# Performance work log

Measured on AMD Instinct MI355X. Metric: run time of the kernel, lower is better.

The kernel has to match this reference:

```python
import jax, jax.numpy as jnp
import numpy as np

N_POINTS = 200
LEVEL_DIM = 4
NUM_LEVELS = 3
RESOLUTIONS = (8, 16, 32)  # base_resolution=8, per-level scale 2
BATCH = 32768


def _sph_to_cart(theta, phi):
    st = jnp.sin(theta)
    return jnp.stack([st * jnp.cos(phi), st * jnp.sin(phi), jnp.cos(theta)], axis=-1)


def _sample_points(x):
    # x: [B,4] -> points on segment between two unit-sphere points: [B, N_POINTS, 3]
    p1 = _sph_to_cart(x[:, 0], x[:, 1])
    p2 = _sph_to_cart(x[:, 2], x[:, 3])
    t = jnp.linspace(0.0, 1.0, N_POINTS, dtype=x.dtype).reshape(1, N_POINTS, 1)
    return p1[:, None, :] + (p2 - p1)[:, None, :] * t


def _grid_interp(points, table, R):
    # points: [B,S,3] in [-1,1]; table: [(R+1)^3, D] dense grid. Trilinear interp.
    u = jnp.clip((points + 1.0) * 0.5, 0.0, 1.0) * R
    p0 = jnp.clip(jnp.floor(u).astype(jnp.int32), 0, R - 1)
    f = u - p0.astype(u.dtype)
    Rp1 = R + 1
    out = jnp.zeros(points.shape[:-1] + (table.shape[-1],), dtype=table.dtype)
    for c in range(8):  # fixed 8 trilinear corners
        off = np.array([(c >> 2) & 1, (c >> 1) & 1, c & 1], dtype=np.int32)
        idx = p0 + off
        lin = (idx[..., 0] * Rp1 + idx[..., 1]) * Rp1 + idx[..., 2]
        w = jnp.prod(jnp.where(off == 1, f, 1.0 - f), axis=-1)
        out = out + w[..., None] * table[lin]
    return out


def setup_inputs() -> dict:
    key = jax.random.key(0)
    ks = jax.random.split(key, 8)
    pi = 3.14159265
    x = jax.random.uniform(ks[0], (BATCH, 4), dtype=jnp.float32) * pi
    grid0 = jax.random.normal(ks[1], ((RESOLUTIONS[0] + 1) ** 3, LEVEL_DIM), jnp.float32) * 0.1
    grid1 = jax.random.normal(ks[2], ((RESOLUTIONS[1] + 1) ** 3, LEVEL_DIM), jnp.float32) * 0.1
    grid2 = jax.random.normal(ks[3], ((RESOLUTIONS[2] + 1) ** 3, LEVEL_DIM), jnp.float32) * 0.1
    w_label = jax.random.normal(ks[4], (NUM_LEVELS, 1), jnp.float32) * 0.5
    b_label = jnp.zeros((1,), jnp.float32)
    w_rgb = jax.random.normal(ks[5], (NUM_LEVELS * (LEVEL_DIM - 1), 3), jnp.float32) * 0.3
    b_rgb = jnp.zeros((3,), jnp.float32)
    return {"x": x, "grid0": grid0, "grid1": grid1, "grid2": grid2,
            "w_label": w_label, "b_label": b_label, "w_rgb": w_rgb, "b_rgb": b_rgb}


def reference(x, grid0, grid1, grid2, w_label, b_label, w_rgb, b_rgb):
    # torch wraps ray sampling in no_grad -> stop_gradient
    points = jax.lax.stop_gradient(_sample_points(x))  # [B,S,3]
    enc = jnp.concatenate(
        [_grid_interp(points, g, R) for g, R in zip((grid0, grid1, grid2), RESOLUTIONS)],
        axis=-1)  # [B,S,12]
    labels_in = enc[:, :, ::LEVEL_DIM]                      # [B,S,3]
    all_prob = jax.nn.sigmoid(labels_in @ w_label + b_label)  # [B,S,1]
    output_hits = jnp.max(all_prob, axis=1)                 # [B,1]
    mask = np.ones(NUM_LEVELS * LEVEL_DIM, dtype=bool)
    mask[::LEVEL_DIM] = False
    rgb_feats = enc[:, :, mask]                             # [B,S,9]
    hit = (all_prob > 0.5).astype(enc.dtype)
    idx_first = jnp.argmax(hit, axis=1)                     # [B,1] first sample with prob>0.5 (0 if none)
    idx3 = jnp.broadcast_to(idx_first[:, :, None], (rgb_feats.shape[0], 1, rgb_feats.shape[2]))
    gathered = jnp.take_along_axis(rgb_feats, idx3, axis=1)[:, 0, :]  # [B,9]
    output_rgb = jax.nn.sigmoid(gathered @ w_rgb + b_rgb)   # [B,3]
    return (output_hits, output_rgb)
```

## Files before the change

### kernel.cpp

```cpp
#include <hip/hip_runtime.h>
#include <math.h>

#define NPTS 200
#define L33   33
#define L33SQ 1089
#define NLAT  35937

template<int R>
__device__ __forceinline__ float tri_label(const float* __restrict__ g,
                                           float ux, float uy, float uz) {
    constexpr int Rp1 = R + 1;
    constexpr int SX  = Rp1 * Rp1;
    int ix = min((int)ux, R - 1);
    int iy = min((int)uy, R - 1);
    int iz = min((int)uz, R - 1);
    float fx = ux - (float)ix, fy = uy - (float)iy, fz = uz - (float)iz;
    int b = (ix * Rp1 + iy) * Rp1 + iz;
    float v000 = g[4*b],            v001 = g[4*(b+1)];
    float v010 = g[4*(b+Rp1)],      v011 = g[4*(b+Rp1+1)];
    float v100 = g[4*(b+SX)],       v101 = g[4*(b+SX+1)];
    float v110 = g[4*(b+SX+Rp1)],   v111 = g[4*(b+SX+Rp1+1)];
    float c00 = fmaf(fz, v001 - v000, v000);
    float c01 = fmaf(fz, v011 - v010, v010);
    float c10 = fmaf(fz, v101 - v100, v100);
    float c11 = fmaf(fz, v111 - v110, v110);
    float c0  = fmaf(fy, c01 - c00, c00);
    float c1  = fmaf(fy, c11 - c10, c10);
    return fmaf(fx, c1 - c0, c0);
}

__device__ __forceinline__ float T_eval(const float* __restrict__ g0,
                                        const float* __restrict__ g1,
                                        const float* __restrict__ g2,
                                        float wl0, float wl1, float wl2, float bl0,
                                        int jx, int jy, int jz) {
    float fx = (float)jx, fy = (float)jy, fz = (float)jz;
    float L0 = tri_label<8 >(g0, fx * 0.25f, fy * 0.25f, fz * 0.25f);
    float L1 = tri_label<16>(g1, fx * 0.5f,  fy * 0.5f,  fz * 0.5f);
    float L2 = g2[4 * ((jx * L33 + jy) * L33 + jz)];
    return bl0 + wl0 * L0 + wl1 * L1 + wl2 * L2;
}

__global__ __launch_bounds__(256)
void prep_kernel(const float* __restrict__ g0, const float* __restrict__ g1,
                 const float* __restrict__ g2, const float* __restrict__ wl,
                 const float* __restrict__ bl, float4* __restrict__ P) {
    int i = blockIdx.x * blockDim.x + threadIdx.x;
    if (i >= NLAT) return;
    int iz = i % L33;
    int r  = i / L33;
    int iy = r % L33;
    int ix = r / L33;
    int izp = min(iz + 1, L33 - 1);
    int iyp = min(iy + 1, L33 - 1);
    float wl0 = wl[0], wl1 = wl[1], wl2 = wl[2], bl0 = bl[0];
    float4 v;
    v.x = T_eval(g0, g1, g2, wl0, wl1, wl2, bl0, ix, iy,  iz );
    v.y = T_eval(g0, g1, g2, wl0, wl1, wl2, bl0, ix, iy,  izp);
    v.z = T_eval(g0, g1, g2, wl0, wl1, wl2, bl0, ix, iyp, iz );
    v.w = T_eval(g0, g1, g2, wl0, wl1, wl2, bl0, ix, iyp, izp);
    P[i] = v;
}

template<int R>
__device__ __forceinline__ void rgb_corner(const float* __restrict__ g,
                                           float cx, float cy, float cz,
                                           int dx, int dy, int dz,
                                           float* f3) {
    constexpr int Rp1 = R + 1;
    float ux = cx * (float)R, uy = cy * (float)R, uz = cz * (float)R;
    int ix = min((int)ux, R - 1);
    int iy = min((int)uy, R - 1);
    int iz = min((int)uz, R - 1);
    float fx = ux - (float)ix, fy = uy - (float)iy, fz = uz - (float)iz;
    int idx = ((ix + dx) * Rp1 + (iy + dy)) * Rp1 + (iz + dz);
    float w = (dx ? fx : 1.0f - fx) * (dy ? fy : 1.0f - fy) * (dz ? fz : 1.0f - fz);
    float4 v = *reinterpret_cast<const float4*>(g + 4 * idx);
    f3[0] = w * v.y;
    f3[1] = w * v.z;
    f3[2] = w * v.w;
}

__global__ __launch_bounds__(256)
void rays_kernel(const float* __restrict__ x,
                 const float4* __restrict__ P,
                 const float* __restrict__ g0,
                 const float* __restrict__ g1,
                 const float* __restrict__ g2,
                 const float* __restrict__ wr,
                 const float* __restrict__ br,
                 float* __restrict__ out_hits,
                 float* __restrict__ out_rgb,
                 int n)
{
    const int tid = blockIdx.x * blockDim.x + threadIdx.x;
    const int ray = tid >> 3;
    const int sub = (int)(threadIdx.x & 7);
    if (ray >= n) return;

    const float th1 = x[ray * 4 + 0];
    const float ph1 = x[ray * 4 + 1];
    const float th2 = x[ray * 4 + 2];
    const float ph2 = x[ray * 4 + 3];
    float s1 = __sinf(th1), c1 = __cosf(th1);
    float s2 = __sinf(th2), c2 = __cosf(th2);
    float p1x = s1 * __cosf(ph1), p1y = s1 * __sinf(ph1), p1z = c1;
    float p2x = s2 * __cosf(ph2), p2y = s2 * __sinf(ph2), p2z = c2;
    const float dxr = p2x - p1x, dyr = p2y - p1y, dzr = p2z - p1z;

    const float inv = 1.0f / (float)(NPTS - 1);
    const float sc  = 16.0f * inv;

    const float bx = fmaf(p1x, 16.0f, 16.0f);
    const float by = fmaf(p1y, 16.0f, 16.0f);
    const float bz = fmaf(p1z, 16.0f, 16.0f);
    const float dux = dxr * sc, duy = dyr * sc, duz = dzr * sc;

    float tf = (float)sub;
    float maxlogit = -INFINITY;
    int firsthit = NPTS;

#pragma unroll 5
    for (int i = 0; i < 25; ++i) {
        float ux = fminf(fmaxf(fmaf(tf, dux, bx), 0.0f), 32.0f);
        float uy = fminf(fmaxf(fmaf(tf, duy, by), 0.0f), 32.0f);
        float uz = fminf(fmaxf(fmaf(tf, duz, bz), 0.0f), 32.0f);
        int ix = min((int)ux, 31);
        int iy = min((int)uy, 31);
        int iz = min((int)uz, 31);
        float fx = ux - (float)ix;
        float fy = uy - (float)iy;
        float fz = uz - (float)iz;
        int idx = (ix * L33 + iy) * L33 + iz;
        float4 q0 = P[idx];
        float4 q1 = P[idx + L33SQ];
        float mx = fmaf(fx, q1.x - q0.x, q0.x);
        float my = fmaf(fx, q1.y - q0.y, q0.y);
        float mz = fmaf(fx, q1.z - q0.z, q0.z);
        float mw = fmaf(fx, q1.w - q0.w, q0.w);
        float r0 = fmaf(fz, my - mx, mx);
        float r1 = fmaf(fz, mw - mz, mz);
        float logit = fmaf(fy, r1 - r0, r0);
        maxlogit = fmaxf(maxlogit, logit);
        if (logit > 0.0f) firsthit = min(firsthit, sub + i * 8);
        tf += 8.0f;
    }

#pragma unroll
    for (int m = 4; m >= 1; m >>= 1) {
        maxlogit = fmaxf(maxlogit, __shfl_xor(maxlogit, m, 64));
        firsthit = min(firsthit, __shfl_xor(firsthit, m, 64));
    }

    const int tsel = (firsthit >= NPTS) ? 0 : firsthit;
    {
        float tt = (float)tsel * inv;
        float px = fmaf(dxr, tt, p1x);
        float py = fmaf(dyr, tt, p1y);
        float pz = fmaf(dzr, tt, p1z);
        float cx = fminf(fmaxf(fmaf(px, 0.5f, 0.5f), 0.0f), 1.0f);
        float cy = fminf(fmaxf(fmaf(py, 0.5f, 0.5f), 0.0f), 1.0f);
        float cz = fminf(fmaxf(fmaf(pz, 0.5f, 0.5f), 0.0f), 1.0f);
        const int dx = (sub >> 2) & 1, dy = (sub >> 1) & 1, dz = sub & 1;
        float feat[9];
        rgb_corner<8 >(g0, cx, cy, cz, dx, dy, dz, &feat[0]);
        rgb_corner<16>(g1, cx, cy, cz, dx, dy, dz, &feat[3]);
        rgb_corner<32>(g2, cx, cy, cz, dx, dy, dz, &feat[6]);
#pragma unroll
        for (int m = 4; m >= 1; m >>= 1) {
#pragma unroll
            for (int k = 0; k < 9; ++k)
                feat[k] += __shfl_xor(feat[k], m, 64);
        }
        if (sub == 0) {
            out_hits[ray] = 1.0f / (1.0f + __expf(-maxlogit));
#pragma unroll
            for (int c = 0; c < 3; ++c) {
                float acc = br[c];
#pragma unroll
                for (int f = 0; f < 9; ++f) acc += feat[f] * wr[f * 3 + c];
                out_rgb[ray * 3 + c] = 1.0f / (1.0f + __expf(-acc));
            }
        }
    }
}

extern "C" void kernel_launch(void* const* d_in, const int* in_sizes, int n_in,
                              void* d_out, int out_size, void* d_ws, size_t ws_size,
                              hipStream_t stream) {
    const float* x  = (const float*)d_in[0];
    const float* g0 = (const float*)d_in[1];
    const float* g1 = (const float*)d_in[2];
    const float* g2 = (const float*)d_in[3];
    const float* wl = (const float*)d_in[4];
    const float* bl = (const float*)d_in[5];
    const float* wr = (const float*)d_in[6];
    const float* br = (const float*)d_in[7];

    const int n = in_sizes[0] / 4;
    float* out_hits = (float*)d_out;
    float* out_rgb  = (float*)d_out + n;

    float4* P = (float4*)d_ws;

    prep_kernel<<<(NLAT + 255) / 256, 256, 0, stream>>>(g0, g1, g2, wl, bl, P);

    const int block = 256;
    const int grid = (n * 8 + block - 1) / block;
    rays_kernel<<<grid, block, 0, stream>>>(x, P, g0, g1, g2, wr, br,
                                            out_hits, out_rgb, n);
}
```

Before: 21.98 us.

## Store 8-corner label cells and give each thread contiguous samples with cell reuse

Label-logit precompute is split into two kernels. The first evaluates the scalar logit per lattice point, removing the 4x redundant evaluation. The second packs all 8 corners of each 32^3 cell into two float4s. The ray kernel now gives each sub-thread 25 contiguous samples instead of strided ones, so consecutive samples usually land in the same cell and the reload is skipped when the cell index is unchanged. This adds a third kernel launch and a divergent branch, and removes the clamp on sample coordinates since points on the unit sphere stay in range.

Measured after the change: 24.75 us. +12.6%, slower.

```diff
diff --git a/kernel.cpp b/kernel.cpp
--- a/kernel.cpp
+++ b/kernel.cpp
@@ -5,6 +5,8 @@
 #define L33   33
 #define L33SQ 1089
 #define NLAT  35937
+#define NCELL 32768
+#define T_OFF_FLOATS (NCELL * 8)
 
 template<int R>
 __device__ __forceinline__ float tri_label(const float* __restrict__ g,
@@ -29,37 +31,38 @@
     return fmaf(fx, c1 - c0, c0);
 }
 
-__device__ __forceinline__ float T_eval(const float* __restrict__ g0,
-                                        const float* __restrict__ g1,
-                                        const float* __restrict__ g2,
-                                        float wl0, float wl1, float wl2, float bl0,
-                                        int jx, int jy, int jz) {
+__global__ __launch_bounds__(256)
+void prep1_kernel(const float* __restrict__ g0, const float* __restrict__ g1,
+                  const float* __restrict__ g2, const float* __restrict__ wl,
+                  const float* __restrict__ bl, float* __restrict__ T) {
+    int i = blockIdx.x * blockDim.x + threadIdx.x;
+    if (i >= NLAT) return;
+    int jz = i % L33;
+    int r  = i / L33;
+    int jy = r % L33;
+    int jx = r / L33;
     float fx = (float)jx, fy = (float)jy, fz = (float)jz;
     float L0 = tri_label<8 >(g0, fx * 0.25f, fy * 0.25f, fz * 0.25f);
     float L1 = tri_label<16>(g1, fx * 0.5f,  fy * 0.5f,  fz * 0.5f);
-    float L2 = g2[4 * ((jx * L33 + jy) * L33 + jz)];
-    return bl0 + wl0 * L0 + wl1 * L1 + wl2 * L2;
+    float L2 = g2[4 * i];
+    T[i] = bl[0] + wl[0] * L0 + wl[1] * L1 + wl[2] * L2;
 }
 
 __global__ __launch_bounds__(256)
-void prep_kernel(const float* __restrict__ g0, const float* __restrict__ g1,
-                 const float* __restrict__ g2, const float* __restrict__ wl,
-                 const float* __restrict__ bl, float4* __restrict__ P) {
+void prep2_kernel(const float* __restrict__ T, float4* __restrict__ C) {
     int i = blockIdx.x * blockDim.x + threadIdx.x;
-    if (i >= NLAT) return;
-    int iz = i % L33;
-    int r  = i / L33;
-    int iy = r % L33;
-    int ix = r / L33;
-    int izp = min(iz + 1, L33 - 1);
-    int iyp = min(iy + 1, L33 - 1);
-    float wl0 = wl[0], wl1 = wl[1], wl2 = wl[2], bl0 = bl[0];
-    float4 v;
-    v.x = T_eval(g0, g1, g2, wl0, wl1, wl2, bl0, ix, iy,  iz );
-    v.y = T_eval(g0, g1, g2, wl0, wl1, wl2, bl0, ix, iy,  izp);
-    v.z = T_eval(g0, g1, g2, wl0, wl1, wl2, bl0, ix, iyp, iz );
-    v.w = T_eval(g0, g1, g2, wl0, wl1, wl2, bl0, ix, iyp, izp);
-    P[i] = v;
+    if (i >= NCELL) return;
+    int iz = i & 31;
+    int iy = (i >> 5) & 31;
+    int ix = i >> 10;
+    int b = (ix * L33 + iy) * L33 + iz;
+    float4 a, c;
+    a.x = T[b];            a.y = T[b + 1];
+    a.z = T[b + L33];      a.w = T[b + L33 + 1];
+    c.x = T[b + L33SQ];        c.y = T[b + L33SQ + 1];
+    c.z = T[b + L33SQ + L33];  c.w = T[b + L33SQ + L33 + 1];
+    C[2 * i]     = a;
+    C[2 * i + 1] = c;
 }
 
 template<int R>
@@ -83,7 +86,7 @@
 
 __global__ __launch_bounds__(256)
 void rays_kernel(const float* __restrict__ x,
-                 const float4* __restrict__ P,
+                 const float4* __restrict__ C,
                  const float* __restrict__ g0,
                  const float* __restrict__ g1,
                  const float* __restrict__ g2,
@@ -116,24 +119,28 @@
     const float bz = fmaf(p1z, 16.0f, 16.0f);
     const float dux = dxr * sc, duy = dyr * sc, duz = dzr * sc;
 
-    float tf = (float)sub;
+    float tf = (float)(sub * 25);
     float maxlogit = -INFINITY;
     int firsthit = NPTS;
-
-#pragma unroll 5
+    int cidx = -1;
+    float4 q0 = {0.f, 0.f, 0.f, 0.f}, q1 = {0.f, 0.f, 0.f, 0.f};
+
     for (int i = 0; i < 25; ++i) {
-        float ux = fminf(fmaxf(fmaf(tf, dux, bx), 0.0f), 32.0f);
-        float uy = fminf(fmaxf(fmaf(tf, duy, by), 0.0f), 32.0f);
-        float uz = fminf(fmaxf(fmaf(tf, duz, bz), 0.0f), 32.0f);
+        float ux = fmaf(tf, dux, bx);
+        float uy = fmaf(tf, duy, by);
+        float uz = fmaf(tf, duz, bz);
         int ix = min((int)ux, 31);
         int iy = min((int)uy, 31);
         int iz = min((int)uz, 31);
         float fx = ux - (float)ix;
         float fy = uy - (float)iy;
         float fz = uz - (float)iz;
-        int idx = (ix * L33 + iy) * L33 + iz;
-        float4 q0 = P[idx];
-        float4 q1 = P[idx + L33SQ];
+        int idx = (ix << 10) + (iy << 5) + iz;
+        if (idx != cidx) {
+            cidx = idx;
+            q0 = C[2 * idx];
+            q1 = C[2 * idx + 1];
+        }
         float mx = fmaf(fx, q1.x - q0.x, q0.x);
         float my = fmaf(fx, q1.y - q0.y, q0.y);
         float mz = fmaf(fx, q1.z - q0.z, q0.z);
@@ -142,8 +149,8 @@
         float r1 = fmaf(fz, mw - mz, mz);
         float logit = fmaf(fy, r1 - r0, r0);
         maxlogit = fmaxf(maxlogit, logit);
-        if (logit > 0.0f) firsthit = min(firsthit, sub + i * 8);
-        tf += 8.0f;
+        if (logit > 0.0f) firsthit = min(firsthit, sub * 25 + i);
+        tf += 1.0f;
     }
 
 #pragma unroll
@@ -201,12 +208,14 @@
     float* out_hits = (float*)d_out;
     float* out_rgb  = (float*)d_out + n;
 
-    float4* P = (float4*)d_ws;
-
-    prep_kernel<<<(NLAT + 255) / 256, 256, 0, stream>>>(g0, g1, g2, wl, bl, P);
+    float4* C = (float4*)d_ws;
+    float*  T = (float*)d_ws + T_OFF_FLOATS;
+
+    prep1_kernel<<<(NLAT + 255) / 256, 256, 0, stream>>>(g0, g1, g2, wl, bl, T);
+    prep2_kernel<<<(NCELL + 255) / 256, 256, 0, stream>>>(T, C);
 
     const int block = 256;
     const int grid = (n * 8 + block - 1) / block;
-    rays_kernel<<<grid, block, 0, stream>>>(x, P, g0, g1, g2, wr, br,
+    rays_kernel<<<grid, block, 0, stream>>>(x, C, g0, g1, g2, wr, br,
                                             out_hits, out_rgb, n);
 }
```

## Reorder precomputed logit lattice x-fastest and reduce rgb after projection

Applied to the files above, without the earlier changes.

The prep kernel now lays out the label-logit lattice with x as the fastest axis and computes one float per thread, so the two corner loads per sample are adjacent float4s instead of a full plane apart. The sample loop is fully unrolled with per-iteration t, the redundant clamps are dropped, and launch bounds request 4 blocks per CU. The rgb path projects the 9 features onto 3 outputs before the cross-lane shuffle, cutting shuffles from 27 to 9. Dropping the clamp assumes the points stay inside [-1,1], which holds for unit-sphere endpoints but could return slightly different indices at exact boundaries.

New measurement: 21.35 us. 1.03x faster.

```diff
diff --git a/kernel.cpp b/kernel.cpp
--- a/kernel.cpp
+++ b/kernel.cpp
@@ -3,8 +3,8 @@
 
 #define NPTS 200
 #define L33   33
-#define L33SQ 1089
 #define NLAT  35937
+#define NPREP (NLAT * 4)
 
 template<int R>
 __device__ __forceinline__ float tri_label(const float* __restrict__ g,
@@ -29,37 +29,25 @@
     return fmaf(fx, c1 - c0, c0);
 }
 
-__device__ __forceinline__ float T_eval(const float* __restrict__ g0,
-                                        const float* __restrict__ g1,
-                                        const float* __restrict__ g2,
-                                        float wl0, float wl1, float wl2, float bl0,
-                                        int jx, int jy, int jz) {
-    float fx = (float)jx, fy = (float)jy, fz = (float)jz;
-    float L0 = tri_label<8 >(g0, fx * 0.25f, fy * 0.25f, fz * 0.25f);
-    float L1 = tri_label<16>(g1, fx * 0.5f,  fy * 0.5f,  fz * 0.5f);
-    float L2 = g2[4 * ((jx * L33 + jy) * L33 + jz)];
-    return bl0 + wl0 * L0 + wl1 * L1 + wl2 * L2;
-}
-
 __global__ __launch_bounds__(256)
 void prep_kernel(const float* __restrict__ g0, const float* __restrict__ g1,
                  const float* __restrict__ g2, const float* __restrict__ wl,
-                 const float* __restrict__ bl, float4* __restrict__ P) {
-    int i = blockIdx.x * blockDim.x + threadIdx.x;
-    if (i >= NLAT) return;
-    int iz = i % L33;
-    int r  = i / L33;
-    int iy = r % L33;
-    int ix = r / L33;
-    int izp = min(iz + 1, L33 - 1);
-    int iyp = min(iy + 1, L33 - 1);
-    float wl0 = wl[0], wl1 = wl[1], wl2 = wl[2], bl0 = bl[0];
-    float4 v;
-    v.x = T_eval(g0, g1, g2, wl0, wl1, wl2, bl0, ix, iy,  iz );
-    v.y = T_eval(g0, g1, g2, wl0, wl1, wl2, bl0, ix, iy,  izp);
-    v.z = T_eval(g0, g1, g2, wl0, wl1, wl2, bl0, ix, iyp, iz );
-    v.w = T_eval(g0, g1, g2, wl0, wl1, wl2, bl0, ix, iyp, izp);
-    P[i] = v;
+                 const float* __restrict__ bl, float* __restrict__ Pf) {
+    int id = blockIdx.x * blockDim.x + threadIdx.x;
+    if (id >= NPREP) return;
+    int c  = id & 3;
+    int jj = id >> 2;
+    int ix = jj % L33;
+    int r  = jj / L33;
+    int iz = r % L33;
+    int iy = r / L33;
+    int jy = min(iy + (c >> 1), L33 - 1);
+    int jz = min(iz + (c & 1),  L33 - 1);
+    float fx = (float)ix, fy = (float)jy, fz = (float)jz;
+    float L0 = tri_label<8 >(g0, fx * 0.25f, fy * 0.25f, fz * 0.25f);
+    float L1 = tri_label<16>(g1, fx * 0.5f,  fy * 0.5f,  fz * 0.5f);
+    float L2 = g2[4 * ((ix * L33 + jy) * L33 + jz)];
+    Pf[id] = bl[0] + wl[0] * L0 + wl[1] * L1 + wl[2] * L2;
 }
 
 template<int R>
@@ -81,7 +69,7 @@
     f3[2] = w * v.w;
 }
 
-__global__ __launch_bounds__(256)
+__global__ __launch_bounds__(256, 4)
 void rays_kernel(const float* __restrict__ x,
                  const float4* __restrict__ P,
                  const float* __restrict__ g0,
@@ -116,24 +104,26 @@
     const float bz = fmaf(p1z, 16.0f, 16.0f);
     const float dux = dxr * sc, duy = dyr * sc, duz = dzr * sc;
 
-    float tf = (float)sub;
+    const float subf = (float)sub;
     float maxlogit = -INFINITY;
     int firsthit = NPTS;
 
-#pragma unroll 5
+#pragma unroll
     for (int i = 0; i < 25; ++i) {
-        float ux = fminf(fmaxf(fmaf(tf, dux, bx), 0.0f), 32.0f);
-        float uy = fminf(fmaxf(fmaf(tf, duy, by), 0.0f), 32.0f);
-        float uz = fminf(fmaxf(fmaf(tf, duz, bz), 0.0f), 32.0f);
+        float tf = subf + (float)(8 * i);
+        float ux = fmaf(tf, dux, bx);
+        float uy = fmaf(tf, duy, by);
+        float uz = fmaf(tf, duz, bz);
         int ix = min((int)ux, 31);
         int iy = min((int)uy, 31);
         int iz = min((int)uz, 31);
         float fx = ux - (float)ix;
         float fy = uy - (float)iy;
         float fz = uz - (float)iz;
-        int idx = (ix * L33 + iy) * L33 + iz;
-        float4 q0 = P[idx];
-        float4 q1 = P[idx + L33SQ];
+        int jj = (iy * L33 + iz) * L33 + ix;
+        const float4* p = P + jj;
+        float4 q0 = p[0];
+        float4 q1 = p[1];
         float mx = fmaf(fx, q1.x - q0.x, q0.x);
         float my = fmaf(fx, q1.y - q0.y, q0.y);
         float mz = fmaf(fx, q1.z - q0.z, q0.z);
@@ -142,8 +132,7 @@
         float r1 = fmaf(fz, mw - mz, mz);
         float logit = fmaf(fy, r1 - r0, r0);
         maxlogit = fmaxf(maxlogit, logit);
-        if (logit > 0.0f) firsthit = min(firsthit, sub + i * 8);
-        tf += 8.0f;
+        if (logit > 0.0f) firsthit = min(firsthit, 8 * i + sub);
     }
 
 #pragma unroll
@@ -166,21 +155,25 @@
         rgb_corner<8 >(g0, cx, cy, cz, dx, dy, dz, &feat[0]);
         rgb_corner<16>(g1, cx, cy, cz, dx, dy, dz, &feat[3]);
         rgb_corner<32>(g2, cx, cy, cz, dx, dy, dz, &feat[6]);
+        float acc[3];
+#pragma unroll
+        for (int c = 0; c < 3; ++c) {
+            float a = 0.0f;
+#pragma unroll
+            for (int f = 0; f < 9; ++f) a = fmaf(feat[f], wr[f * 3 + c], a);
+            acc[c] = a;
+        }
 #pragma unroll
         for (int m = 4; m >= 1; m >>= 1) {
 #pragma unroll
-            for (int k = 0; k < 9; ++k)
-                feat[k] += __shfl_xor(feat[k], m, 64);
+            for (int c = 0; c < 3; ++c)
+                acc[c] += __shfl_xor(acc[c], m, 64);
         }
         if (sub == 0) {
             out_hits[ray] = 1.0f / (1.0f + __expf(-maxlogit));
 #pragma unroll
-            for (int c = 0; c < 3; ++c) {
-                float acc = br[c];
-#pragma unroll
-                for (int f = 0; f < 9; ++f) acc += feat[f] * wr[f * 3 + c];
-                out_rgb[ray * 3 + c] = 1.0f / (1.0f + __expf(-acc));
-            }
+            for (int c = 0; c < 3; ++c)
+                out_rgb[ray * 3 + c] = 1.0f / (1.0f + __expf(-(acc[c] + br[c])));
         }
     }
 }
@@ -201,12 +194,12 @@
     float* out_hits = (float*)d_out;
     float* out_rgb  = (float*)d_out + n;
 
-    float4* P = (float4*)d_ws;
-
-    prep_kernel<<<(NLAT + 255) / 256, 256, 0, stream>>>(g0, g1, g2, wl, bl, P);
+    float* Pf = (float*)d_ws;
+
+    prep_kernel<<<(NPREP + 255) / 256, 256, 0, stream>>>(g0, g1, g2, wl, bl, Pf);
 
     const int block = 256;
     const int grid = (n * 8 + block - 1) / block;
-    rays_kernel<<<grid, block, 0, stream>>>(x, P, g0, g1, g2, wr, br,
-                                            out_hits, out_rgb, n);
-}
+    rays_kernel<<<grid, block, 0, stream>>>(x, (const float4*)Pf, g0, g1, g2,
+                                            wr, br, out_hits, out_rgb, n);
+}
```
